# Performance work log

Measured on AMD Instinct MI355X. Metric: run time of the kernel, lower is better.

## Reference

```python
import jax, jax.numpy as jnp
import numpy as np

D = 128      # d_feat / d_model
L = 512      # seq_len
H = 8        # heads (hardcoded in FourierBlock weights)
E = D // H   # head dim = 16
MODES = 64   # low-frequency modes (mode_select='low' -> index = range(MODES))
MA = 25      # moving_avg kernel
NL = 2       # e_layers
DFF = 512
EPS = 1e-5


def _positional(length, dim):
    pos = jnp.arange(length, dtype=jnp.float32)[:, None]
    div = jnp.exp(jnp.arange(0, dim, 2, dtype=jnp.float32) * (-np.log(10000.0) / dim))
    pe = jnp.zeros((length, dim), dtype=jnp.float32)
    pe = pe.at[:, 0::2].set(jnp.sin(pos * div))
    pe = pe.at[:, 1::2].set(jnp.cos(pos * div))
    return pe


def _mov_mean(x, k):
    # series_decomp moving average: replicate-pad (k-1)//2 each side, window mean stride 1
    pad = (k - 1) // 2
    xp = jnp.concatenate([jnp.repeat(x[:, :1], pad, axis=1), x,
                          jnp.repeat(x[:, -1:], pad, axis=1)], axis=1)
    cs = jnp.cumsum(xp, axis=1)
    cs = jnp.concatenate([jnp.zeros_like(cs[:, :1]), cs], axis=1)
    return (cs[:, k:] - cs[:, :-k]) / k


def _fourier_layer(x, Wq, bq, Wo, bo, fwr, fwi):
    # AutoCorrelationLayer(query proj -> FourierBlock -> out proj); k/v projections are unused by FourierBlock
    B = x.shape[0]
    q = (x @ Wq + bq).reshape(B, L, H, E).transpose(0, 2, 3, 1)   # B,H,E,L
    xft = jnp.fft.rfft(q, axis=-1)                                # B,H,E,L//2+1
    Wc = fwr + 1j * fwi                                           # H,E,E,M (complex mode weights)
    sel = jnp.einsum('bhem,heom->bhom', xft[..., :MODES], Wc)
    out_ft = jnp.zeros((B, H, E, L // 2 + 1), dtype=sel.dtype).at[..., :MODES].set(sel)
    y = jnp.fft.irfft(out_ft, n=L, axis=-1)                       # B,H,E,L
    y = y.reshape(B, L, H * E)  # matches torch .view(B, L, -1) on contiguous B,H,E,L
    return y @ Wo + bo


def _enc_layer(x, Wq, bq, Wo, bo, fwr, fwi, W1, W2):
    x = x + _fourier_layer(x, Wq, bq, Wo, bo, fwr, fwi)
    x = x - _mov_mean(x, MA)                                  # decomp1 seasonal part
    y = jax.nn.gelu(x @ W1, approximate=False) @ W2           # 1x1 convs == matmuls, no bias
    s = x + y
    return s - _mov_mean(s, MA)                               # decomp2 seasonal part


def setup_inputs() -> dict:
    key = jax.random.key(0)
    ks = jax.random.split(key, 12)
    B = 128
    scale = 1.0 / (D * D)
    return {
        "x_enc": jax.random.normal(ks[0], (B, D * L), dtype=jnp.float32),
        "x_mark_enc": jax.random.uniform(ks[1], (B, D * L), dtype=jnp.float32),
        "x_dec": jnp.zeros((1,), jnp.float32),
        "x_mark_dec": jnp.zeros((1,), jnp.float32),
        "conv_w": jax.random.normal(ks[2], (D, D, 3), dtype=jnp.float32) * 0.02,
        "Wq": jax.random.normal(ks[3], (NL, D, D), dtype=jnp.float32) * 0.02,
        "bq": jnp.zeros((NL, D), jnp.float32),
        "Wo": jax.random.normal(ks[4], (NL, D, D), dtype=jnp.float32) * 0.02,
        "bo": jnp.zeros((NL, D), jnp.float32),
        "fwr": jax.random.uniform(ks[5], (NL, H, E, E, MODES), dtype=jnp.float32) * scale,
        "fwi": jax.random.uniform(ks[6], (NL, H, E, E, MODES), dtype=jnp.float32) * scale,
        "W1": jax.random.normal(ks[7], (NL, D, DFF), dtype=jnp.float32) * 0.02,
        "W2": jax.random.normal(ks[8], (NL, DFF, D), dtype=jnp.float32) * 0.02,
        "ln_g": jnp.ones((D,), jnp.float32),
        "ln_b": jnp.zeros((D,), jnp.float32),
        "proj_w": jax.random.normal(ks[9], (D * L,), dtype=jnp.float32) * 0.002,
        "proj_b": jnp.zeros((), jnp.float32),
    }


def reference(x_enc, x_mark_enc, x_dec, x_mark_dec, conv_w, Wq, bq, Wo, bo,
              fwr, fwi, W1, W2, ln_g, ln_b, proj_w, proj_b):
    B = x_enc.shape[0]
    x = x_enc.reshape(B, D, L).transpose(0, 2, 1)          # B,L,D
    mark = x_mark_enc.reshape(B, D, L).transpose(0, 2, 1)  # B,L,D
    # TokenEmbedding: Conv1d kernel 3, circular padding, no bias
    xc = x.transpose(0, 2, 1)                              # B,D,L
    xp = jnp.concatenate([xc[:, :, -1:], xc, xc[:, :, :1]], axis=-1)
    tok = jax.lax.conv_general_dilated(xp, conv_w, (1,), 'VALID',
                                       dimension_numbers=('NCH', 'OIH', 'NCH'))
    h = tok.transpose(0, 2, 1) + _positional(L, D)[None]   # + sinusoidal PE (dropout=0)
    for l in range(NL):
        h = _enc_layer(h, Wq[l], bq[l], Wo[l], bo[l], fwr[l], fwi[l], W1[l], W2[l])
    # my_Layernorm: LayerNorm over features, then subtract mean over time axis
    mu = h.mean(-1, keepdims=True)
    var = h.var(-1, keepdims=True)
    hn = (h - mu) / jnp.sqrt(var + EPS) * ln_g + ln_b
    hn = hn - hn.mean(axis=1, keepdims=True)
    o = jax.nn.gelu(hn, approximate=False) * mark          # act + mask-mul
    return o.reshape(B, -1) @ proj_w + proj_b              # (B,) after squeeze
```

## Files before the change

### kernel.cpp

```cpp
#include <hip/hip_runtime.h>
#include <math.h>

#define DFF 512
#define NLAYER 2

typedef __bf16 bf16x8 __attribute__((ext_vector_type(8)));
typedef float f32x4 __attribute__((ext_vector_type(4)));

__device__ __forceinline__ float4 f4_load(const float* p) { return *(const float4*)p; }
__device__ __forceinline__ void f4_store(float* p, float4 v) { *(float4*)p = v; }
__device__ __forceinline__ float4 f4_zero() { return make_float4(0.f, 0.f, 0.f, 0.f); }
__device__ __forceinline__ void f4_fma(float4& a, float s, const float4 w) {
    a.x += s * w.x; a.y += s * w.y; a.z += s * w.z; a.w += s * w.w;
}
__device__ __forceinline__ float gelu_f(float x) {
    return 0.5f * x * (1.0f + erff(x * 0.70710678118654752440f));
}
__device__ __forceinline__ int sw_off(int r, int c) {
    return (r << 7) + (((c >> 3) ^ (r & 7)) << 3) + (c & 7);
}
__device__ __forceinline__ void store_bf4(__bf16* p, float4 v) {
    __bf16 t[4] = {(__bf16)v.x, (__bf16)v.y, (__bf16)v.z, (__bf16)v.w};
    *(uint2*)p = *(uint2*)t;
}

__global__ __launch_bounds__(256) void k_init(float* __restrict__ pe,
                                              float* __restrict__ Ftt,
                                              float* __restrict__ G) {
    int idx = blockIdx.x * 256 + threadIdx.x;
    {
        int l = idx >> 7, d = idx & 127;
        int j = d >> 1;
        double div = exp((double)(2 * j) * (-log(10000.0) / 128.0));
        double a = (double)l * div;
        pe[idx] = (d & 1) ? (float)cos(a) : (float)sin(a);
    }
    {
        int m2 = idx >> 9, t = idx & 511;
        int m = m2 >> 1;
        int r = (m * t) & 511;
        double ang = (double)r * (6.283185307179586476925287 / 512.0);
        float cv = (float)cos(ang), sv = (float)sin(ang);
        float f = (m2 & 1) ? -sv : cv;
        Ftt[idx] = f;
        float s = (m == 0) ? (1.0f / 512.0f) : (2.0f / 512.0f);
        G[idx] = f * s;
    }
}

__global__ __launch_bounds__(256) void k_castw(const float* __restrict__ Wq,
                                               const float* __restrict__ Wo,
                                               const float* __restrict__ W1,
                                               const float* __restrict__ W2,
                                               const float* __restrict__ cw,
                                               __bf16* __restrict__ wbf,
                                               __bf16* __restrict__ cwtk) {
    int i = blockIdx.x * 256 + threadIdx.x;
    if (i < 65536) {
        int r = i & 16383, l = (i >> 14) & 1;
        int n = r >> 7, k = r & 127;
        const float* W = (i >= 32768) ? Wo : Wq;
        wbf[i] = (__bf16)W[l * 16384 + k * 128 + n];
    } else if (i < 196608) {
        int j = i - 65536;
        int l = j >> 16, r = j & 65535;
        int f = r >> 7, k = r & 127;
        wbf[i] = (__bf16)W1[l * 65536 + k * 512 + f];
    } else if (i < 327680) {
        int j = i - 196608;
        int l = j >> 16, r = j & 65535;
        int n = r >> 9, f = r & 511;
        wbf[i] = (__bf16)W2[l * 65536 + f * 128 + n];
    } else if (i < 376832) {
        int j = i - 327680;
        int s = j >> 14, r = j & 16383;
        int d = r >> 7, ii = r & 127;
        cwtk[j] = (__bf16)cw[(d * 128 + ii) * 3 + s];
    }
}

__global__ __launch_bounds__(256) void k_xpose(const float* __restrict__ xe,
                                               __bf16* __restrict__ xt) {
    __shared__ float ts[128][65];
    const int b = blockIdx.y, l0 = blockIdx.x * 64;
    for (int idx = threadIdx.x; idx < 128 * 16; idx += 256) {
        int d = idx >> 4, c4 = idx & 15;
        float4 v = f4_load(&xe[((size_t)b * 128 + d) * 512 + l0 + c4 * 4]);
        ts[d][c4 * 4 + 0] = v.x; ts[d][c4 * 4 + 1] = v.y;
        ts[d][c4 * 4 + 2] = v.z; ts[d][c4 * 4 + 3] = v.w;
    }
    __syncthreads();
#pragma unroll
    for (int p = 0; p < 4; ++p) {
        int l = (threadIdx.x >> 4) + p * 16;
        int d0 = (threadIdx.x & 15) * 8;
        __bf16 tmp[8];
#pragma unroll
        for (int j = 0; j < 8; ++j) tmp[j] = (__bf16)ts[d0 + j][l];
        *(uint4*)&xt[((size_t)b * 512 + l0 + l) * 128 + d0] = *(uint4*)tmp;
    }
}

__global__ __launch_bounds__(256) void k_embed_m(const __bf16* __restrict__ xt,
                                                 const __bf16* __restrict__ cwtk,
                                                 const float* __restrict__ pe,
                                                 float* __restrict__ h,
                                                 __bf16* __restrict__ hb) {
    __shared__ __align__(16) __bf16 xs[130 * 128];
    const int b = blockIdx.x >> 2, l0 = (blockIdx.x & 3) * 128;
    for (int c = threadIdx.x; c < 130 * 16; c += 256) {
        int r = c >> 4, g = c & 15;
        int gl = (l0 - 1 + r) & 511;
        *(uint4*)&xs[(r << 7) + ((g ^ (r & 7)) << 3)] =
            *(const uint4*)&xt[(((size_t)b * 512 + gl) << 7) + (g << 3)];
    }
    __syncthreads();
    const int lane = threadIdx.x & 63, wid = threadIdx.x >> 6;
    const int wrow = (wid & 1) * 64, wcol = (wid >> 1) * 64;
    const int m16 = lane & 15, quad = lane >> 4;
    f32x4 acc[4][4];
#pragma unroll
    for (int a = 0; a < 4; ++a)
#pragma unroll
        for (int bb = 0; bb < 4; ++bb) acc[a][bb] = {0.f, 0.f, 0.f, 0.f};
#pragma unroll
    for (int s = 0; s < 3; ++s) {
#pragma unroll
        for (int ks = 0; ks < 4; ++ks) {
            const int ko = ks * 32 + quad * 8;
            bf16x8 af[4], bfr[4];
#pragma unroll
            for (int rt = 0; rt < 4; ++rt) {
                int r = wrow + rt * 16 + m16 + s;
                af[rt] = *(const bf16x8*)&xs[(r << 7) + (((ks * 4 + quad) ^ (r & 7)) << 3)];
            }
#pragma unroll
            for (int ct = 0; ct < 4; ++ct)
                bfr[ct] = *(const bf16x8*)&cwtk[((size_t)(s * 128 + wcol + ct * 16 + m16) << 7) + ko];
#pragma unroll
            for (int rt = 0; rt < 4; ++rt)
#pragma unroll
                for (int ct = 0; ct < 4; ++ct)
                    acc[rt][ct] = __builtin_amdgcn_mfma_f32_16x16x32_bf16(
                        af[rt], bfr[ct], acc[rt][ct], 0, 0, 0);
        }
    }
#pragma unroll
    for (int ct = 0; ct < 4; ++ct) {
        int gcol = wcol + ct * 16 + m16;
#pragma unroll
        for (int rt = 0; rt < 4; ++rt)
#pragma unroll
            for (int r = 0; r < 4; ++r) {
                int l = l0 + wrow + rt * 16 + quad * 4 + r;
                float v = acc[rt][ct][r] + pe[l * 128 + gcol];
                size_t gi = (((size_t)b * 512 + l) << 7) + gcol;
                h[gi] = v;
                hb[gi] = (__bf16)v;
            }
    }
}

template <bool RES>
__global__ __launch_bounds__(256) void k_mgemm(const __bf16* __restrict__ Xb,
                                               const __bf16* __restrict__ Wt,
                                               const float* __restrict__ bias,
                                               const float* __restrict__ R,
                                               float* __restrict__ out) {
    __shared__ __align__(16) __bf16 xs[128 * 128];
    const int rowBase = blockIdx.x * 128;
#pragma unroll
    for (int i = 0; i < 8; ++i) {
        int c = i * 256 + threadIdx.x;
        int r = c >> 4, g = c & 15;
        *(uint4*)&xs[(r << 7) + ((g ^ (r & 7)) << 3)] =
            *(const uint4*)&Xb[(((size_t)rowBase + r) << 7) + (g << 3)];
    }
    __syncthreads();
    const int lane = threadIdx.x & 63, wid = threadIdx.x >> 6;
    const int wrow = (wid & 1) * 64, wcol = (wid >> 1) * 64;
    const int m16 = lane & 15, quad = lane >> 4;
    f32x4 acc[4][4];
#pragma unroll
    for (int a = 0; a < 4; ++a)
#pragma unroll
        for (int b = 0; b < 4; ++b) acc[a][b] = {0.f, 0.f, 0.f, 0.f};
#pragma unroll
    for (int ks = 0; ks < 4; ++ks) {
        const int ko = ks * 32 + quad * 8;
        const int xg = (((ks * 4 + quad) ^ (m16 & 7)) << 3);
        bf16x8 af[4], bfr[4];
#pragma unroll
        for (int rt = 0; rt < 4; ++rt)
            af[rt] = *(const bf16x8*)&xs[((wrow + rt * 16 + m16) << 7) + xg];
#pragma unroll
        for (int ct = 0; ct < 4; ++ct)
            bfr[ct] = *(const bf16x8*)&Wt[((size_t)(wcol + ct * 16 + m16) << 7) + ko];
#pragma unroll
        for (int rt = 0; rt < 4; ++rt)
#pragma unroll
            for (int ct = 0; ct < 4; ++ct)
                acc[rt][ct] = __builtin_amdgcn_mfma_f32_16x16x32_bf16(
                    af[rt], bfr[ct], acc[rt][ct], 0, 0, 0);
    }
#pragma unroll
    for (int ct = 0; ct < 4; ++ct) {
        int gcol = wcol + ct * 16 + m16;
        float bv = bias[gcol];
#pragma unroll
        for (int rt = 0; rt < 4; ++rt)
#pragma unroll
            for (int r = 0; r < 4; ++r) {
                size_t gi = ((size_t)(rowBase + wrow + rt * 16 + quad * 4 + r) << 7) + gcol;
                float v = acc[rt][ct][r] + bv;
                if (RES) v += R[gi];
                out[gi] = v;
            }
    }
}

__global__ __launch_bounds__(256) void k_ffnm(const __bf16* __restrict__ Xb,
                                              const float* __restrict__ Xf,
                                              const __bf16* __restrict__ W1t,
                                              const __bf16* __restrict__ W2t,
                                              float* __restrict__ out) {
    __shared__ __align__(16) __bf16 xs[128 * 128];
    __shared__ __align__(16) __bf16 ts[128 * 128];
    const int rowBase = blockIdx.x * 128;
#pragma unroll
    for (int i = 0; i < 8; ++i) {
        int c = i * 256 + threadIdx.x;
        int r = c >> 4, g = c & 15;
        *(uint4*)&xs[(r << 7) + ((g ^ (r & 7)) << 3)] =
            *(const uint4*)&Xb[(((size_t)rowBase + r) << 7) + (g << 3)];
    }
    __syncthreads();
    const int lane = threadIdx.x & 63, wid = threadIdx.x >> 6;
    const int wrow = (wid & 1) * 64, wcol = (wid >> 1) * 64;
    const int m16 = lane & 15, quad = lane >> 4;
    f32x4 acc2[4][4];
#pragma unroll
    for (int a = 0; a < 4; ++a)
#pragma unroll
        for (int b = 0; b < 4; ++b) acc2[a][b] = {0.f, 0.f, 0.f, 0.f};

    for (int f0 = 0; f0 < DFF; f0 += 128) {
        f32x4 c1[4][4];
#pragma unroll
        for (int a = 0; a < 4; ++a)
#pragma unroll
            for (int b = 0; b < 4; ++b) c1[a][b] = {0.f, 0.f, 0.f, 0.f};
#pragma unroll
        for (int ks = 0; ks < 4; ++ks) {
            const int ko = ks * 32 + quad * 8;
            const int xg = (((ks * 4 + quad) ^ (m16 & 7)) << 3);
            bf16x8 af[4], bfr[4];
#pragma unroll
            for (int rt = 0; rt < 4; ++rt)
                af[rt] = *(const bf16x8*)&xs[((wrow + rt * 16 + m16) << 7) + xg];
#pragma unroll
            for (int ct = 0; ct < 4; ++ct)
                bfr[ct] = *(const bf16x8*)&W1t[((size_t)(f0 + wcol + ct * 16 + m16) << 7) + ko];
#pragma unroll
            for (int rt = 0; rt < 4; ++rt)
#pragma unroll
                for (int ct = 0; ct < 4; ++ct)
                    c1[rt][ct] = __builtin_amdgcn_mfma_f32_16x16x32_bf16(
                        af[rt], bfr[ct], c1[rt][ct], 0, 0, 0);
        }
#pragma unroll
        for (int rt = 0; rt < 4; ++rt)
#pragma unroll
            for (int ct = 0; ct < 4; ++ct)
#pragma unroll
                for (int r = 0; r < 4; ++r) {
                    int lrow = wrow + rt * 16 + quad * 4 + r;
                    int lcol = wcol + ct * 16 + m16;
                    ts[sw_off(lrow, lcol)] = (__bf16)gelu_f(c1[rt][ct][r]);
                }
        __syncthreads();
#pragma unroll
        for (int ks = 0; ks < 4; ++ks) {
            const int ko = ks * 32 + quad * 8;
            const int xg = (((ks * 4 + quad) ^ (m16 & 7)) << 3);
            bf16x8 af[4], bfr[4];
#pragma unroll
            for (int rt = 0; rt < 4; ++rt)
                af[rt] = *(const bf16x8*)&ts[((wrow + rt * 16 + m16) << 7) + xg];
#pragma unroll
            for (int ct = 0; ct < 4; ++ct)
                bfr[ct] = *(const bf16x8*)&W2t[((size_t)(wcol + ct * 16 + m16) << 9) + f0 + ko];
#pragma unroll
            for (int rt = 0; rt < 4; ++rt)
#pragma unroll
                for (int ct = 0; ct < 4; ++ct)
                    acc2[rt][ct] = __builtin_amdgcn_mfma_f32_16x16x32_bf16(
                        af[rt], bfr[ct], acc2[rt][ct], 0, 0, 0);
        }
        __syncthreads();
    }
#pragma unroll
    for (int ct = 0; ct < 4; ++ct) {
        int gcol = wcol + ct * 16 + m16;
#pragma unroll
        for (int rt = 0; rt < 4; ++rt)
#pragma unroll
            for (int r = 0; r < 4; ++r) {
                size_t gi = ((size_t)(rowBase + wrow + rt * 16 + quad * 4 + r) << 7) + gcol;
                out[gi] = acc2[rt][ct][r] + Xf[gi];
            }
    }
}

__global__ __launch_bounds__(256) void k_fdft(const float* __restrict__ q,
                                              const float* __restrict__ Ftt,
                                              float* __restrict__ cbuf) {
    __shared__ float fs[32][512];
    const int b = blockIdx.y, m2b = blockIdx.x * 32;
    for (int idx = threadIdx.x; idx < 32 * 128; idx += 256) {
        int r = idx >> 7, c4 = idx & 127;
        f4_store(&fs[r][c4 * 4], f4_load(&Ftt[(m2b + r) * 512 + c4 * 4]));
    }
    __syncthreads();
    const int dg = threadIdx.x & 31, mg = threadIdx.x >> 5;
    const int d0 = dg * 4, m0 = mg * 4;
    float4 acc4[4];
#pragma unroll
    for (int m = 0; m < 4; ++m) acc4[m] = f4_zero();
    for (int t = 0; t < 512; t += 4) {
        float4 q0 = f4_load(&q[((size_t)b * 512 + t + 0) * 128 + d0]);
        float4 q1 = f4_load(&q[((size_t)b * 512 + t + 1) * 128 + d0]);
        float4 q2 = f4_load(&q[((size_t)b * 512 + t + 2) * 128 + d0]);
        float4 q3 = f4_load(&q[((size_t)b * 512 + t + 3) * 128 + d0]);
#pragma unroll
        for (int mj = 0; mj < 4; ++mj) {
            float4 f = f4_load(&fs[m0 + mj][t]);
            f4_fma(acc4[mj], f.x, q0); f4_fma(acc4[mj], f.y, q1);
            f4_fma(acc4[mj], f.z, q2); f4_fma(acc4[mj], f.w, q3);
        }
    }
    f4_store(&cbuf[((size_t)b * 128 + d0 + 0) * 128 + m2b + m0],
             make_float4(acc4[0].x, acc4[1].x, acc4[2].x, acc4[3].x));
    f4_store(&cbuf[((size_t)b * 128 + d0 + 1) * 128 + m2b + m0],
             make_float4(acc4[0].y, acc4[1].y, acc4[2].y, acc4[3].y));
    f4_store(&cbuf[((size_t)b * 128 + d0 + 2) * 128 + m2b + m0],
             make_float4(acc4[0].z, acc4[1].z, acc4[2].z, acc4[3].z));
    f4_store(&cbuf[((size_t)b * 128 + d0 + 3) * 128 + m2b + m0],
             make_float4(acc4[0].w, acc4[1].w, acc4[2].w, acc4[3].w));
}

__global__ __launch_bounds__(256) void k_mix(const float* __restrict__ cbuf,
                                             const float* __restrict__ fwr,
                                             const float* __restrict__ fwi,
                                             float* __restrict__ dd) {
    __shared__ float cs[16][128];
    const int hh = blockIdx.x, b = blockIdx.y;
    for (int idx = threadIdx.x; idx < 16 * 32; idx += 256) {
        int e = idx >> 5, c4 = idx & 31;
        f4_store(&cs[e][c4 * 4],
                 f4_load(&cbuf[((size_t)b * 128 + hh * 16 + e) * 128 + c4 * 4]));
    }
    __syncthreads();
    const int m = threadIdx.x & 63, og = threadIdx.x >> 6;
    float dr[4] = {0.f, 0.f, 0.f, 0.f}, di[4] = {0.f, 0.f, 0.f, 0.f};
    for (int e = 0; e < 16; ++e) {
        float2 cv = *(const float2*)&cs[e][2 * m];
#pragma unroll
        for (int oi = 0; oi < 4; ++oi) {
            int o = og * 4 + oi;
            float wr = fwr[(((size_t)hh * 16 + e) * 16 + o) * 64 + m];
            float wi = fwi[(((size_t)hh * 16 + e) * 16 + o) * 64 + m];
            dr[oi] += cv.x * wr - cv.y * wi;
            di[oi] += cv.x * wi + cv.y * wr;
        }
    }
#pragma unroll
    for (int oi = 0; oi < 4; ++oi) {
        int o = og * 4 + oi;
        float2 v = make_float2(dr[oi], di[oi]);
        *(float2*)&dd[((size_t)b * 128 + hh * 16 + o) * 128 + 2 * m] = v;
    }
}

__global__ __launch_bounds__(256) void k_idft(const float* __restrict__ dd,
                                              const float* __restrict__ G,
                                              __bf16* __restrict__ y) {
    __shared__ float ds[128][65];
    const int b = blockIdx.y, t0 = blockIdx.x * 64;
    const int hog = threadIdx.x & 31, tg = threadIdx.x >> 5;
    const int tb = tg * 8;
    float4 acc4[8];
#pragma unroll
    for (int t = 0; t < 8; ++t) acc4[t] = f4_zero();
    for (int half = 0; half < 2; ++half) {
        if (half) __syncthreads();
        for (int idx = threadIdx.x; idx < 128 * 16; idx += 256) {
            int ho = idx >> 4, c4 = idx & 15;
            float4 v = f4_load(&dd[((size_t)b * 128 + ho) * 128 + half * 64 + c4 * 4]);
            ds[ho][c4 * 4 + 0] = v.x; ds[ho][c4 * 4 + 1] = v.y;
            ds[ho][c4 * 4 + 2] = v.z; ds[ho][c4 * 4 + 3] = v.w;
        }
        __syncthreads();
        for (int m2l = 0; m2l < 64; ++m2l) {
            int m2 = half * 64 + m2l;
            float4 dvec = make_float4(ds[hog][m2l], ds[hog + 32][m2l],
                                      ds[hog + 64][m2l], ds[hog + 96][m2l]);
            float4 g0 = f4_load(&G[(size_t)m2 * 512 + t0 + tb]);
            float4 g1 = f4_load(&G[(size_t)m2 * 512 + t0 + tb + 4]);
            f4_fma(acc4[0], g0.x, dvec); f4_fma(acc4[1], g0.y, dvec);
            f4_fma(acc4[2], g0.z, dvec); f4_fma(acc4[3], g0.w, dvec);
            f4_fma(acc4[4], g1.x, dvec); f4_fma(acc4[5], g1.y, dvec);
            f4_fma(acc4[6], g1.z, dvec); f4_fma(acc4[7], g1.w, dvec);
        }
    }
#pragma unroll
    for (int hj = 0; hj < 4; ++hj) {
        __bf16 tmp[8];
#pragma unroll
        for (int ti = 0; ti < 8; ++ti) {
            float v = (hj == 0) ? acc4[ti].x : (hj == 1) ? acc4[ti].y
                    : (hj == 2) ? acc4[ti].z : acc4[ti].w;
            tmp[ti] = (__bf16)v;
        }
        *(uint4*)&y[((size_t)b * 128 + hog + hj * 32) * 512 + t0 + tb] = *(uint4*)tmp;
    }
}

__global__ __launch_bounds__(256) void k_decomp(const float* __restrict__ X,
                                                float* __restrict__ out,
                                                __bf16* __restrict__ outb) {
    __shared__ float xs[88][128];
    const int b = blockIdx.y, l0 = blockIdx.x * 64;
    for (int idx = threadIdx.x; idx < 88 * 32; idx += 256) {
        int r = idx >> 5, c4 = idx & 31;
        int gl = l0 - 12 + r;
        gl = gl < 0 ? 0 : (gl > 511 ? 511 : gl);
        f4_store(&xs[r][c4 * 4], f4_load(&X[((size_t)b * 512 + gl) * 128 + c4 * 4]));
    }
    __syncthreads();
    const int dg = threadIdx.x & 31, lg = threadIdx.x >> 5;
    const int d0 = dg * 4, base = lg * 8;
    float4 s = f4_zero();
#pragma unroll
    for (int w = 0; w < 25; ++w) {
        float4 v = f4_load(&xs[base + w][d0]);
        s.x += v.x; s.y += v.y; s.z += v.z; s.w += v.w;
    }
    const float inv = 1.0f / 25.0f;
#pragma unroll
    for (int i = 0; i < 8; ++i) {
        int t = base + 12 + i;
        float4 x = f4_load(&xs[t][d0]);
        float4 o = make_float4(x.x - s.x * inv, x.y - s.y * inv,
                               x.z - s.z * inv, x.w - s.w * inv);
        size_t gi = ((size_t)b * 512 + l0 + lg * 8 + i) * 128 + d0;
        f4_store(&out[gi], o);
        store_bf4(&outb[gi], o);
        if (i < 7) {
            float4 a = f4_load(&xs[base + 25 + i][d0]);
            float4 r = f4_load(&xs[base + i][d0]);
            s.x += a.x - r.x; s.y += a.y - r.y; s.z += a.z - r.z; s.w += a.w - r.w;
        }
    }
}

__global__ __launch_bounds__(256) void k_ln(const float* __restrict__ X,
                                            const float* __restrict__ g,
                                            const float* __restrict__ bb,
                                            float* __restrict__ out) {
    const int row = blockIdx.x * 4 + (threadIdx.x >> 6);
    const int lane = threadIdx.x & 63;
    float2 v = *(const float2*)&X[(size_t)row * 128 + lane * 2];
    float s = v.x + v.y, ss = v.x * v.x + v.y * v.y;
#pragma unroll
    for (int o = 32; o; o >>= 1) {
        s += __shfl_xor(s, o);
        ss += __shfl_xor(ss, o);
    }
    float mu = s * (1.0f / 128.0f);
    float var = ss * (1.0f / 128.0f) - mu * mu;
    float rstd = rsqrtf(var + 1e-5f);
    float2 gg = *(const float2*)&g[lane * 2];
    float2 bv = *(const float2*)&bb[lane * 2];
    float2 o;
    o.x = (v.x - mu) * rstd * gg.x + bv.x;
    o.y = (v.y - mu) * rstd * gg.y + bv.y;
    *(float2*)&out[(size_t)row * 128 + lane * 2] = o;
}

__global__ __launch_bounds__(128) void k_colmean(const float* __restrict__ X,
                                                 float* __restrict__ cm) {
    const int b = blockIdx.y, l0 = blockIdx.x * 64, d = threadIdx.x;
    float s = 0.f;
    for (int l = l0; l < l0 + 64; ++l) s += X[((size_t)b * 512 + l) * 128 + d];
    atomicAdd(&cm[b * 128 + d], s);
}

__global__ __launch_bounds__(128) void k_final(const float* __restrict__ hn,
                                               const float* __restrict__ cm,
                                               const float* __restrict__ mark,
                                               const float* __restrict__ pw,
                                               const float* __restrict__ pb,
                                               float* __restrict__ out) {
    const int b = blockIdx.y, l0 = blockIdx.x * 128, d = threadIdx.x;
    const float c = cm[b * 128 + d] * (1.0f / 512.0f);
    float acc = 0.f;
    for (int l = l0; l < l0 + 128; ++l) {
        float v = hn[((size_t)b * 512 + l) * 128 + d] - c;
        acc += gelu_f(v) * mark[((size_t)b * 128 + d) * 512 + l] * pw[l * 128 + d];
    }
    __shared__ float red[2];
#pragma unroll
    for (int o = 32; o; o >>= 1) acc += __shfl_xor(acc, o);
    if ((threadIdx.x & 63) == 0) red[threadIdx.x >> 6] = acc;
    __syncthreads();
    if (threadIdx.x == 0) {
        float tot = red[0] + red[1];
        if (blockIdx.x == 0) tot += pb[0];
        atomicAdd(&out[b], tot);
    }
}

extern "C" void kernel_launch(void* const* d_in, const int* in_sizes, int n_in,
                              void* d_out, int out_size, void* d_ws, size_t ws_size,
                              hipStream_t stream) {
    const float* xe   = (const float*)d_in[0];
    const float* mark = (const float*)d_in[1];
    const float* cw   = (const float*)d_in[4];
    const float* Wq   = (const float*)d_in[5];
    const float* bq   = (const float*)d_in[6];
    const float* Wo   = (const float*)d_in[7];
    const float* bo   = (const float*)d_in[8];
    const float* fwr  = (const float*)d_in[9];
    const float* fwi  = (const float*)d_in[10];
    const float* W1   = (const float*)d_in[11];
    const float* W2   = (const float*)d_in[12];
    const float* lng  = (const float*)d_in[13];
    const float* lnb  = (const float*)d_in[14];
    const float* pw   = (const float*)d_in[15];
    const float* pb   = (const float*)d_in[16];
    float* out = (float*)d_out;

    float* ws   = (float*)d_ws;
    float* Ftt  = ws;
    float* G    = ws + 65536;
    float* h    = ws + 131072;
    float* bufA = ws + 8519680;
    __bf16* hb  = (__bf16*)(ws + 16908288);
    float* yrg  = ws + 21102592;
    float* cm   = ws + 25296896;
    __bf16* wbf = (__bf16*)(ws + 25313280);
    float* pe   = yrg;
    __bf16* cwtk = (__bf16*)(yrg + 65536);
    float* cbuf = yrg;
    __bf16* yb  = (__bf16*)yrg;
    __bf16* xt  = (__bf16*)bufA;
    __bf16* Wqt = wbf;
    __bf16* Wot = wbf + 32768;
    __bf16* W1t = wbf + 65536;
    __bf16* W2t = wbf + 196608;

    k_init<<<256, 256, 0, stream>>>(pe, Ftt, G);
    k_castw<<<1472, 256, 0, stream>>>(Wq, Wo, W1, W2, cw, wbf, cwtk);
    k_xpose<<<dim3(8, 128), 256, 0, stream>>>(xe, xt);
    k_embed_m<<<512, 256, 0, stream>>>(xt, cwtk, pe, h, hb);
    for (int l = 0; l < NLAYER; ++l) {
        k_mgemm<false><<<512, 256, 0, stream>>>(hb, Wqt + l * 16384, bq + l * 128,
                                                nullptr, bufA);
        k_fdft<<<dim3(4, 128), 256, 0, stream>>>(bufA, Ftt, cbuf);
        k_mix<<<dim3(8, 128), 256, 0, stream>>>(cbuf, fwr + l * 131072,
                                                fwi + l * 131072, bufA);
        k_idft<<<dim3(8, 128), 256, 0, stream>>>(bufA, G, yb);
        k_mgemm<true><<<512, 256, 0, stream>>>(yb, Wot + l * 16384, bo + l * 128,
                                               h, bufA);
        k_decomp<<<dim3(8, 128), 256, 0, stream>>>(bufA, h, hb);
        k_ffnm<<<512, 256, 0, stream>>>(hb, h, W1t + l * 65536, W2t + l * 65536, bufA);
        k_decomp<<<dim3(8, 128), 256, 0, stream>>>(bufA, h, hb);
    }
    k_ln<<<16384, 256, 0, stream>>>(h, lng, lnb, bufA);
    hipMemsetAsync(cm, 0, 16384 * sizeof(float), stream);
    k_colmean<<<dim3(8, 128), 128, 0, stream>>>(bufA, cm);
    hipMemsetAsync(d_out, 0, 128 * sizeof(float), stream);
    k_final<<<dim3(4, 128), 128, 0, stream>>>(bufA, cm, mark, pw, pb, out);

    (void)in_sizes; (void)n_in; (void)out_size; (void)ws_size;
}
```

Baseline: 742.1 us.

## Move forward and inverse DFT onto bf16 MFMA with transposed q projection

Replaces the fp32 scalar DFT and inverse-DFT kernels with bf16 MFMA GEMM kernels. The query projection now writes a transposed bf16 layout so the forward DFT reads contiguous time rows, and the mixing step emits bf16 for the inverse GEMM. The DFT twiddle tables become bf16 and the inverse table is transposed. The FFN intermediate shared buffer also switches from an XOR swizzle to a padded leading dimension read with split 64-bit loads. The goal is to cut the FP32 ALU cost of the spectral step, at the price of bf16 rounding in the DFT stages and some strided global stores.

```diff
diff --git a/kernel.cpp b/kernel.cpp
--- a/kernel.cpp
+++ b/kernel.cpp
@@ -3,8 +3,10 @@
 
 #define DFF 512
 #define NLAYER 2
+#define TS_LD 132
 
 typedef __bf16 bf16x8 __attribute__((ext_vector_type(8)));
+typedef __bf16 bf16x4 __attribute__((ext_vector_type(4)));
 typedef float f32x4 __attribute__((ext_vector_type(4)));
 
 __device__ __forceinline__ float4 f4_load(const float* p) { return *(const float4*)p; }
@@ -16,17 +18,19 @@
 __device__ __forceinline__ float gelu_f(float x) {
     return 0.5f * x * (1.0f + erff(x * 0.70710678118654752440f));
 }
-__device__ __forceinline__ int sw_off(int r, int c) {
-    return (r << 7) + (((c >> 3) ^ (r & 7)) << 3) + (c & 7);
-}
 __device__ __forceinline__ void store_bf4(__bf16* p, float4 v) {
     __bf16 t[4] = {(__bf16)v.x, (__bf16)v.y, (__bf16)v.z, (__bf16)v.w};
     *(uint2*)p = *(uint2*)t;
 }
+__device__ __forceinline__ bf16x8 ld_b64x2(const __bf16* p) {
+    bf16x4 lo = *(const bf16x4*)p;
+    bf16x4 hi = *(const bf16x4*)(p + 4);
+    return __builtin_shufflevector(lo, hi, 0, 1, 2, 3, 4, 5, 6, 7);
+}
 
 __global__ __launch_bounds__(256) void k_init(float* __restrict__ pe,
-                                              float* __restrict__ Ftt,
-                                              float* __restrict__ G) {
+                                              __bf16* __restrict__ Fttb,
+                                              __bf16* __restrict__ Gtb) {
     int idx = blockIdx.x * 256 + threadIdx.x;
     {
         int l = idx >> 7, d = idx & 127;
@@ -42,9 +46,9 @@
         double ang = (double)r * (6.283185307179586476925287 / 512.0);
         float cv = (float)cos(ang), sv = (float)sin(ang);
         float f = (m2 & 1) ? -sv : cv;
-        Ftt[idx] = f;
+        Fttb[idx] = (__bf16)f;
         float s = (m == 0) ? (1.0f / 512.0f) : (2.0f / 512.0f);
-        G[idx] = f * s;
+        Gtb[t * 128 + m2] = (__bf16)(f * s);
     }
 }
 
@@ -161,6 +165,176 @@
     }
 }
 
+__global__ __launch_bounds__(256) void k_qprojT(const __bf16* __restrict__ Xb,
+                                                const __bf16* __restrict__ Wt,
+                                                const float* __restrict__ bias,
+                                                __bf16* __restrict__ qT) {
+    __shared__ __align__(16) __bf16 xs[128 * 128];
+    const int rowBase = blockIdx.x * 128;
+#pragma unroll
+    for (int i = 0; i < 8; ++i) {
+        int c = i * 256 + threadIdx.x;
+        int r = c >> 4, g = c & 15;
+        *(uint4*)&xs[(r << 7) + ((g ^ (r & 7)) << 3)] =
+            *(const uint4*)&Xb[(((size_t)rowBase + r) << 7) + (g << 3)];
+    }
+    __syncthreads();
+    const int lane = threadIdx.x & 63, wid = threadIdx.x >> 6;
+    const int wn = (wid & 1) * 64, wr = (wid >> 1) * 64;
+    const int m16 = lane & 15, quad = lane >> 4;
+    f32x4 acc[4][4];
+#pragma unroll
+    for (int a = 0; a < 4; ++a)
+#pragma unroll
+        for (int b = 0; b < 4; ++b) acc[a][b] = {0.f, 0.f, 0.f, 0.f};
+#pragma unroll
+    for (int ks = 0; ks < 4; ++ks) {
+        const int ko = ks * 32 + quad * 8;
+        bf16x8 wf[4], xf[4];
+#pragma unroll
+        for (int rt = 0; rt < 4; ++rt)
+            wf[rt] = *(const bf16x8*)&Wt[((size_t)(wn + rt * 16 + m16) << 7) + ko];
+#pragma unroll
+        for (int ct = 0; ct < 4; ++ct) {
+            int r = wr + ct * 16 + m16;
+            xf[ct] = *(const bf16x8*)&xs[(r << 7) + (((ks * 4 + quad) ^ (r & 7)) << 3)];
+        }
+#pragma unroll
+        for (int rt = 0; rt < 4; ++rt)
+#pragma unroll
+            for (int ct = 0; ct < 4; ++ct)
+                acc[rt][ct] = __builtin_amdgcn_mfma_f32_16x16x32_bf16(
+                    wf[rt], xf[ct], acc[rt][ct], 0, 0, 0);
+    }
+#pragma unroll
+    for (int rt = 0; rt < 4; ++rt)
+#pragma unroll
+        for (int r = 0; r < 4; ++r) {
+            int n = wn + rt * 16 + quad * 4 + r;
+            float bv = bias[n];
+#pragma unroll
+            for (int ct = 0; ct < 4; ++ct) {
+                int grow = rowBase + wr + ct * 16 + m16;
+                qT[(size_t)n * 65536 + grow] = (__bf16)(acc[rt][ct][r] + bv);
+            }
+        }
+}
+
+__global__ __launch_bounds__(128) void k_fdft_m(const __bf16* __restrict__ qT,
+                                                const __bf16* __restrict__ Fttb,
+                                                float* __restrict__ c) {
+    const int b = blockIdx.y, d0 = blockIdx.x * 64;
+    const int lane = threadIdx.x & 63, wid = threadIdx.x >> 6;
+    const int wm = wid * 64;
+    const int m16 = lane & 15, quad = lane >> 4;
+    f32x4 acc[4][4];
+#pragma unroll
+    for (int a = 0; a < 4; ++a)
+#pragma unroll
+        for (int bb = 0; bb < 4; ++bb) acc[a][bb] = {0.f, 0.f, 0.f, 0.f};
+    for (int ks = 0; ks < 16; ++ks) {
+        const int ko = ks * 32 + quad * 8;
+        bf16x8 af[4], bf[4];
+#pragma unroll
+        for (int rt = 0; rt < 4; ++rt)
+            af[rt] = *(const bf16x8*)&qT[(size_t)(d0 + rt * 16 + m16) * 65536 + b * 512 + ko];
+#pragma unroll
+        for (int ct = 0; ct < 4; ++ct)
+            bf[ct] = *(const bf16x8*)&Fttb[(size_t)(wm + ct * 16 + m16) * 512 + ko];
+#pragma unroll
+        for (int rt = 0; rt < 4; ++rt)
+#pragma unroll
+            for (int ct = 0; ct < 4; ++ct)
+                acc[rt][ct] = __builtin_amdgcn_mfma_f32_16x16x32_bf16(
+                    af[rt], bf[ct], acc[rt][ct], 0, 0, 0);
+    }
+#pragma unroll
+    for (int ct = 0; ct < 4; ++ct) {
+        int m2 = wm + ct * 16 + m16;
+#pragma unroll
+        for (int rt = 0; rt < 4; ++rt)
+#pragma unroll
+            for (int r = 0; r < 4; ++r) {
+                int d = d0 + rt * 16 + quad * 4 + r;
+                c[((size_t)b * 128 + d) * 128 + m2] = acc[rt][ct][r];
+            }
+    }
+}
+
+__global__ __launch_bounds__(256) void k_mix(const float* __restrict__ cbuf,
+                                             const float* __restrict__ fwr,
+                                             const float* __restrict__ fwi,
+                                             __bf16* __restrict__ ddb) {
+    __shared__ float cs[16][128];
+    const int hh = blockIdx.x, b = blockIdx.y;
+    for (int idx = threadIdx.x; idx < 16 * 32; idx += 256) {
+        int e = idx >> 5, c4 = idx & 31;
+        f4_store(&cs[e][c4 * 4],
+                 f4_load(&cbuf[((size_t)b * 128 + hh * 16 + e) * 128 + c4 * 4]));
+    }
+    __syncthreads();
+    const int m = threadIdx.x & 63, og = threadIdx.x >> 6;
+    float dr[4] = {0.f, 0.f, 0.f, 0.f}, di[4] = {0.f, 0.f, 0.f, 0.f};
+    for (int e = 0; e < 16; ++e) {
+        float2 cv = *(const float2*)&cs[e][2 * m];
+#pragma unroll
+        for (int oi = 0; oi < 4; ++oi) {
+            int o = og * 4 + oi;
+            float wr = fwr[(((size_t)hh * 16 + e) * 16 + o) * 64 + m];
+            float wi = fwi[(((size_t)hh * 16 + e) * 16 + o) * 64 + m];
+            dr[oi] += cv.x * wr - cv.y * wi;
+            di[oi] += cv.x * wi + cv.y * wr;
+        }
+    }
+#pragma unroll
+    for (int oi = 0; oi < 4; ++oi) {
+        int o = og * 4 + oi;
+        __bf16 t2[2] = {(__bf16)dr[oi], (__bf16)di[oi]};
+        *(uint*)&ddb[((size_t)b * 128 + hh * 16 + o) * 128 + 2 * m] = *(uint*)t2;
+    }
+}
+
+__global__ __launch_bounds__(256) void k_idft_m(const __bf16* __restrict__ ddb,
+                                                const __bf16* __restrict__ Gtb,
+                                                __bf16* __restrict__ y) {
+    const int b = blockIdx.y, t0 = blockIdx.x * 128;
+    const int lane = threadIdx.x & 63, wid = threadIdx.x >> 6;
+    const int wt = (wid & 1) * 64, wh = (wid >> 1) * 64;
+    const int m16 = lane & 15, quad = lane >> 4;
+    f32x4 acc[4][4];
+#pragma unroll
+    for (int a = 0; a < 4; ++a)
+#pragma unroll
+        for (int bb = 0; bb < 4; ++bb) acc[a][bb] = {0.f, 0.f, 0.f, 0.f};
+#pragma unroll
+    for (int ks = 0; ks < 4; ++ks) {
+        const int ko = ks * 32 + quad * 8;
+        bf16x8 af[4], bf[4];
+#pragma unroll
+        for (int rt = 0; rt < 4; ++rt)
+            af[rt] = *(const bf16x8*)&Gtb[(size_t)(t0 + wt + rt * 16 + m16) * 128 + ko];
+#pragma unroll
+        for (int ct = 0; ct < 4; ++ct)
+            bf[ct] = *(const bf16x8*)&ddb[((size_t)b * 128 + wh + ct * 16 + m16) * 128 + ko];
+#pragma unroll
+        for (int rt = 0; rt < 4; ++rt)
+#pragma unroll
+            for (int ct = 0; ct < 4; ++ct)
+                acc[rt][ct] = __builtin_amdgcn_mfma_f32_16x16x32_bf16(
+                    af[rt], bf[ct], acc[rt][ct], 0, 0, 0);
+    }
+#pragma unroll
+    for (int rt = 0; rt < 4; ++rt)
+#pragma unroll
+        for (int ct = 0; ct < 4; ++ct) {
+            int ho = wh + ct * 16 + m16;
+            int tb = t0 + wt + rt * 16 + quad * 4;
+            __bf16 tmp[4] = {(__bf16)acc[rt][ct][0], (__bf16)acc[rt][ct][1],
+                             (__bf16)acc[rt][ct][2], (__bf16)acc[rt][ct][3]};
+            *(uint2*)&y[((size_t)b * 128 + ho) * 512 + tb] = *(uint2*)tmp;
+        }
+}
+
 template <bool RES>
 __global__ __launch_bounds__(256) void k_mgemm(const __bf16* __restrict__ Xb,
                                                const __bf16* __restrict__ Wt,
@@ -225,7 +399,7 @@
                                               const __bf16* __restrict__ W2t,
                                               float* __restrict__ out) {
     __shared__ __align__(16) __bf16 xs[128 * 128];
-    __shared__ __align__(16) __bf16 ts[128 * 128];
+    __shared__ __align__(16) __bf16 ts[128 * TS_LD];
     const int rowBase = blockIdx.x * 128;
 #pragma unroll
     for (int i = 0; i < 8; ++i) {
@@ -276,17 +450,16 @@
                 for (int r = 0; r < 4; ++r) {
                     int lrow = wrow + rt * 16 + quad * 4 + r;
                     int lcol = wcol + ct * 16 + m16;
-                    ts[sw_off(lrow, lcol)] = (__bf16)gelu_f(c1[rt][ct][r]);
+                    ts[lrow * TS_LD + lcol] = (__bf16)gelu_f(c1[rt][ct][r]);
                 }
         __syncthreads();
 #pragma unroll
         for (int ks = 0; ks < 4; ++ks) {
             const int ko = ks * 32 + quad * 8;
-            const int xg = (((ks * 4 + quad) ^ (m16 & 7)) << 3);
             bf16x8 af[4], bfr[4];
 #pragma unroll
             for (int rt = 0; rt < 4; ++rt)
-                af[rt] = *(const bf16x8*)&ts[((wrow + rt * 16 + m16) << 7) + xg];
+                af[rt] = ld_b64x2(&ts[(wrow + rt * 16 + m16) * TS_LD + ko]);
 #pragma unroll
             for (int ct = 0; ct < 4; ++ct)
                 bfr[ct] = *(const bf16x8*)&W2t[((size_t)(wcol + ct * 16 + m16) << 9) + f0 + ko];
@@ -309,120 +482,6 @@
                 size_t gi = ((size_t)(rowBase + wrow + rt * 16 + quad * 4 + r) << 7) + gcol;
                 out[gi] = acc2[rt][ct][r] + Xf[gi];
             }
-    }
-}
-
-__global__ __launch_bounds__(256) void k_fdft(const float* __restrict__ q,
-                                              const float* __restrict__ Ftt,
-                                              float* __restrict__ cbuf) {
-    __shared__ float fs[32][512];
-    const int b = blockIdx.y, m2b = blockIdx.x * 32;
-    for (int idx = threadIdx.x; idx < 32 * 128; idx += 256) {
-        int r = idx >> 7, c4 = idx & 127;
-        f4_store(&fs[r][c4 * 4], f4_load(&Ftt[(m2b + r) * 512 + c4 * 4]));
-    }
-    __syncthreads();
-    const int dg = threadIdx.x & 31, mg = threadIdx.x >> 5;
-    const int d0 = dg * 4, m0 = mg * 4;
-    float4 acc4[4];
-#pragma unroll
-    for (int m = 0; m < 4; ++m) acc4[m] = f4_zero();
-    for (int t = 0; t < 512; t += 4) {
-        float4 q0 = f4_load(&q[((size_t)b * 512 + t + 0) * 128 + d0]);
-        float4 q1 = f4_load(&q[((size_t)b * 512 + t + 1) * 128 + d0]);
-        float4 q2 = f4_load(&q[((size_t)b * 512 + t + 2) * 128 + d0]);
-        float4 q3 = f4_load(&q[((size_t)b * 512 + t + 3) * 128 + d0]);
-#pragma unroll
-        for (int mj = 0; mj < 4; ++mj) {
-            float4 f = f4_load(&fs[m0 + mj][t]);
-            f4_fma(acc4[mj], f.x, q0); f4_fma(acc4[mj], f.y, q1);
-            f4_fma(acc4[mj], f.z, q2); f4_fma(acc4[mj], f.w, q3);
-        }
-    }
-    f4_store(&cbuf[((size_t)b * 128 + d0 + 0) * 128 + m2b + m0],
-             make_float4(acc4[0].x, acc4[1].x, acc4[2].x, acc4[3].x));
-    f4_store(&cbuf[((size_t)b * 128 + d0 + 1) * 128 + m2b + m0],
-             make_float4(acc4[0].y, acc4[1].y, acc4[2].y, acc4[3].y));
-    f4_store(&cbuf[((size_t)b * 128 + d0 + 2) * 128 + m2b + m0],
-             make_float4(acc4[0].z, acc4[1].z, acc4[2].z, acc4[3].z));
-    f4_store(&cbuf[((size_t)b * 128 + d0 + 3) * 128 + m2b + m0],
-             make_float4(acc4[0].w, acc4[1].w, acc4[2].w, acc4[3].w));
-}
-
-__global__ __launch_bounds__(256) void k_mix(const float* __restrict__ cbuf,
-                                             const float* __restrict__ fwr,
-                                             const float* __restrict__ fwi,
-                                             float* __restrict__ dd) {
-    __shared__ float cs[16][128];
-    const int hh = blockIdx.x, b = blockIdx.y;
-    for (int idx = threadIdx.x; idx < 16 * 32; idx += 256) {
-        int e = idx >> 5, c4 = idx & 31;
-        f4_store(&cs[e][c4 * 4],
-                 f4_load(&cbuf[((size_t)b * 128 + hh * 16 + e) * 128 + c4 * 4]));
-    }
-    __syncthreads();
-    const int m = threadIdx.x & 63, og = threadIdx.x >> 6;
-    float dr[4] = {0.f, 0.f, 0.f, 0.f}, di[4] = {0.f, 0.f, 0.f, 0.f};
-    for (int e = 0; e < 16; ++e) {
-        float2 cv = *(const float2*)&cs[e][2 * m];
-#pragma unroll
-        for (int oi = 0; oi < 4; ++oi) {
-            int o = og * 4 + oi;
-            float wr = fwr[(((size_t)hh * 16 + e) * 16 + o) * 64 + m];
-            float wi = fwi[(((size_t)hh * 16 + e) * 16 + o) * 64 + m];
-            dr[oi] += cv.x * wr - cv.y * wi;
-            di[oi] += cv.x * wi + cv.y * wr;
-        }
-    }
-#pragma unroll
-    for (int oi = 0; oi < 4; ++oi) {
-        int o = og * 4 + oi;
-        float2 v = make_float2(dr[oi], di[oi]);
-        *(float2*)&dd[((size_t)b * 128 + hh * 16 + o) * 128 + 2 * m] = v;
-    }
-}
-
-__global__ __launch_bounds__(256) void k_idft(const float* __restrict__ dd,
-                                              const float* __restrict__ G,
-                                              __bf16* __restrict__ y) {
-    __shared__ float ds[128][65];
-    const int b = blockIdx.y, t0 = blockIdx.x * 64;
-    const int hog = threadIdx.x & 31, tg = threadIdx.x >> 5;
-    const int tb = tg * 8;
-    float4 acc4[8];
-#pragma unroll
-    for (int t = 0; t < 8; ++t) acc4[t] = f4_zero();
-    for (int half = 0; half < 2; ++half) {
-        if (half) __syncthreads();
-        for (int idx = threadIdx.x; idx < 128 * 16; idx += 256) {
-            int ho = idx >> 4, c4 = idx & 15;
-            float4 v = f4_load(&dd[((size_t)b * 128 + ho) * 128 + half * 64 + c4 * 4]);
-            ds[ho][c4 * 4 + 0] = v.x; ds[ho][c4 * 4 + 1] = v.y;
-            ds[ho][c4 * 4 + 2] = v.z; ds[ho][c4 * 4 + 3] = v.w;
-        }
-        __syncthreads();
-        for (int m2l = 0; m2l < 64; ++m2l) {
-            int m2 = half * 64 + m2l;
-            float4 dvec = make_float4(ds[hog][m2l], ds[hog + 32][m2l],
-                                      ds[hog + 64][m2l], ds[hog + 96][m2l]);
-            float4 g0 = f4_load(&G[(size_t)m2 * 512 + t0 + tb]);
-            float4 g1 = f4_load(&G[(size_t)m2 * 512 + t0 + tb + 4]);
-            f4_fma(acc4[0], g0.x, dvec); f4_fma(acc4[1], g0.y, dvec);
-            f4_fma(acc4[2], g0.z, dvec); f4_fma(acc4[3], g0.w, dvec);
-            f4_fma(acc4[4], g1.x, dvec); f4_fma(acc4[5], g1.y, dvec);
-            f4_fma(acc4[6], g1.z, dvec); f4_fma(acc4[7], g1.w, dvec);
-        }
-    }
-#pragma unroll
-    for (int hj = 0; hj < 4; ++hj) {
-        __bf16 tmp[8];
-#pragma unroll
-        for (int ti = 0; ti < 8; ++ti) {
-            float v = (hj == 0) ? acc4[ti].x : (hj == 1) ? acc4[ti].y
-                    : (hj == 2) ? acc4[ti].z : acc4[ti].w;
-            tmp[ti] = (__bf16)v;
-        }
-        *(uint4*)&y[((size_t)b * 128 + hog + hj * 32) * 512 + t0 + tb] = *(uint4*)tmp;
     }
 }
 
@@ -541,36 +600,37 @@
     const float* pb   = (const float*)d_in[16];
     float* out = (float*)d_out;
 
-    float* ws   = (float*)d_ws;
-    float* Ftt  = ws;
-    float* G    = ws + 65536;
-    float* h    = ws + 131072;
-    float* bufA = ws + 8519680;
-    __bf16* hb  = (__bf16*)(ws + 16908288);
-    float* yrg  = ws + 21102592;
-    float* cm   = ws + 25296896;
-    __bf16* wbf = (__bf16*)(ws + 25313280);
-    float* pe   = yrg;
+    float* ws    = (float*)d_ws;
+    __bf16* Fttb = (__bf16*)ws;
+    __bf16* Gtb  = (__bf16*)(ws + 65536);
+    float* h     = ws + 131072;
+    float* bufA  = ws + 8519680;
+    __bf16* hb   = (__bf16*)(ws + 16908288);
+    float* yrg   = ws + 21102592;
+    float* cm    = ws + 25296896;
+    __bf16* wbf  = (__bf16*)(ws + 25313280);
+    float* pe    = yrg;
     __bf16* cwtk = (__bf16*)(yrg + 65536);
-    float* cbuf = yrg;
-    __bf16* yb  = (__bf16*)yrg;
-    __bf16* xt  = (__bf16*)bufA;
-    __bf16* Wqt = wbf;
-    __bf16* Wot = wbf + 32768;
-    __bf16* W1t = wbf + 65536;
-    __bf16* W2t = wbf + 196608;
-
-    k_init<<<256, 256, 0, stream>>>(pe, Ftt, G);
+    float* cbuf  = yrg;
+    __bf16* yb   = (__bf16*)yrg;
+    __bf16* xt   = (__bf16*)bufA;
+    __bf16* qT   = (__bf16*)bufA;
+    __bf16* ddb  = (__bf16*)(bufA + 4194304);
+    __bf16* Wqt  = wbf;
+    __bf16* Wot  = wbf + 32768;
+    __bf16* W1t  = wbf + 65536;
+    __bf16* W2t  = wbf + 196608;
+
+    k_init<<<256, 256, 0, stream>>>(pe, Fttb, Gtb);
     k_castw<<<1472, 256, 0, stream>>>(Wq, Wo, W1, W2, cw, wbf, cwtk);
     k_xpose<<<dim3(8, 128), 256, 0, stream>>>(xe, xt);
     k_embed_m<<<512, 256, 0, stream>>>(xt, cwtk, pe, h, hb);
     for (int l = 0; l < NLAYER; ++l) {
-        k_mgemm<false><<<512, 256, 0, stream>>>(hb, Wqt + l * 16384, bq + l * 128,
-                                                nullptr, bufA);
-        k_fdft<<<dim3(4, 128), 256, 0, stream>>>(bufA, Ftt, cbuf);
+        k_qprojT<<<512, 256, 0, stream>>>(hb, Wqt + l * 16384, bq + l * 128, qT);
+        k_fdft_m<<<dim3(2, 128), 128, 0, stream>>>(qT, Fttb, cbuf);
         k_mix<<<dim3(8, 128), 256, 0, stream>>>(cbuf, fwr + l * 131072,
-                                                fwi + l * 131072, bufA);
-        k_idft<<<dim3(8, 128), 256, 0, stream>>>(bufA, G, yb);
+                                                fwi + l * 131072, ddb);
+        k_idft_m<<<dim3(4, 128), 256, 0, stream>>>(ddb, Gtb, yb);
         k_mgemm<true><<<512, 256, 0, stream>>>(yb, Wot + l * 16384, bo + l * 128,
                                                h, bufA);
         k_decomp<<<dim3(8, 128), 256, 0, stream>>>(bufA, h, hb);
```

New measurement: 658.5 us. -11.3%, faster.
